# Kernel tuning notes

Measured on AMD Instinct MI355X. Metric: run time of the kernel, lower is better.

The kernel has to match this reference:

```python
import jax, jax.numpy as jnp
import numpy as np

N_NODES = 50000
N_EDGES = 800000
D_IN = 128
D_OUT = 128


def setup_inputs() -> dict:
    key = jax.random.key(0)
    k1, k2, k3, k4 = jax.random.split(key, 4)
    node_features = jax.random.normal(k1, (N_NODES, D_IN), dtype=jnp.float32)
    edge_index = jax.random.randint(k2, (2, N_EDGES), 0, N_NODES, dtype=jnp.int64)
    # nn.Linear params: weight [out, in], bias [out]
    W = jax.random.normal(k3, (D_OUT, D_IN), dtype=jnp.float32) / np.sqrt(D_IN)
    b = jax.random.normal(k4, (D_OUT,), dtype=jnp.float32) * 0.01
    return {"node_features": node_features, "edge_index": edge_index, "W": W, "b": b}


def reference(node_features, edge_index, W, b):
    source_nodes = edge_index[0]
    dest_nodes = edge_index[1]
    # gather neighbor features [E, D_in], scatter-add into [N, D_in]
    neighbor_features = node_features[source_nodes]
    aggregated = jax.ops.segment_sum(neighbor_features, dest_nodes,
                                     num_segments=node_features.shape[0])
    # nn.Linear: x @ W.T + b
    return aggregated @ W.T + b
```

## Files before the change

### kernel.cpp

```cpp
#include <hip/hip_runtime.h>


constexpr int NN = 50000;
constexpr int NE = 800000;
constexpr int D  = 128;

constexpr int BS  = 128;
constexpr int NB  = (NN + BS - 1) / BS;
constexpr int CAP = 4096;
constexpr int EPB = 4096;
constexpr int NBLK_B = (NE + EPB - 1) / EPB;

constexpr int AROWU = 136;

typedef __attribute__((ext_vector_type(8))) short bf16x8;
typedef __attribute__((ext_vector_type(4))) float f32x4;

__device__ inline unsigned short f2bf(float f) {
    unsigned u = __float_as_uint(f);
    return (unsigned short)((u + 0x7fffu + ((u >> 16) & 1u)) >> 16);
}
__device__ inline float bflo(unsigned v) { return __uint_as_float(v << 16); }
__device__ inline float bfhi(unsigned v) { return __uint_as_float(v & 0xffff0000u); }

constexpr int NF4 = NN * D / 4;
constexpr int W4  = D * D / 4;
constexpr int NBLK_P = (NF4 + W4 + 255) / 256;
constexpr int GRID_A = NBLK_B + NBLK_P;

__global__ __launch_bounds__(256) void k_prep_bucket(
    const float* __restrict__ nf, const float* __restrict__ W,
    const int* __restrict__ ei,
    ushort* __restrict__ nfh, ushort* __restrict__ Wh,
    int* __restrict__ cursor, unsigned* __restrict__ buf)
{
    __shared__ int h[NB];
    __shared__ int gbase[NB];
    __shared__ int lcur[NB];
    const int t = threadIdx.x;

    if (blockIdx.x < NBLK_B) {
        for (int i = t; i < NB; i += 256) { h[i] = 0; lcur[i] = 0; }
        __syncthreads();
        const int e0 = blockIdx.x * EPB;
        unsigned pk[16];
        #pragma unroll
        for (int j = 0; j < 16; ++j) {
            int e = e0 + j * 256 + t;
            if (e < NE) {
                unsigned s = (unsigned)ei[e];
                unsigned d = (unsigned)ei[NE + e];
                pk[j] = (d << 16) | s;
                atomicAdd(&h[pk[j] >> 23], 1);
            }
        }
        __syncthreads();
        for (int i = t; i < NB; i += 256)
            if (h[i] > 0) gbase[i] = i * CAP + atomicAdd(&cursor[i], h[i]);
        __syncthreads();
        #pragma unroll
        for (int j = 0; j < 16; ++j) {
            int e = e0 + j * 256 + t;
            if (e < NE) {
                unsigned b = pk[j] >> 23;
                int l = atomicAdd(&lcur[b], 1);
                buf[gbase[b] + l] = pk[j];
            }
        }
    } else {
        int i = (blockIdx.x - NBLK_B) * 256 + t;
        if (i < NF4) {
            float4 v = ((const float4*)nf)[i];
            ((ushort4*)nfh)[i] = make_ushort4(f2bf(v.x), f2bf(v.y), f2bf(v.z), f2bf(v.w));
        } else if (i < NF4 + W4) {
            int k = i - NF4;
            float4 v = ((const float4*)W)[k];
            ((ushort4*)Wh)[k] = make_ushort4(f2bf(v.x), f2bf(v.y), f2bf(v.z), f2bf(v.w));
        }
    }
}

__global__ __launch_bounds__(1024) void k_sort_agg(
    const unsigned* __restrict__ nfh, const unsigned* __restrict__ buf,
    const int* __restrict__ cursor, const ushort* __restrict__ Wh,
    const float* __restrict__ bias, float* __restrict__ out)
{
    __shared__ ushort srt[CAP];
    __shared__ int hist[BS], off[BS], cur[BS];
    __shared__ unsigned tile[BS * AROWU / 2];
    const int b = blockIdx.x, t = threadIdx.x;
    const int lane = t & 63, w = t >> 6;

    int cnt = cursor[b]; if (cnt > CAP) cnt = CAP;
    const unsigned* mybuf = buf + (size_t)b * CAP;

    if (t < BS) hist[t] = 0;
    __syncthreads();
    for (int e = t; e < cnt; e += 1024)
        atomicAdd(&hist[(mybuf[e] >> 16) & (BS - 1)], 1);
    __syncthreads();
    if (t < BS) off[t] = hist[t];
    __syncthreads();
    for (int o = 1; o < BS; o <<= 1) {
        int v = (t >= o && t < BS) ? off[t - o] : 0;
        __syncthreads();
        if (t < BS) off[t] += v;
        __syncthreads();
    }
    if (t < BS) { int ex = off[t] - hist[t]; off[t] = ex; cur[t] = ex; }
    __syncthreads();
    for (int e = t; e < cnt; e += 1024) {
        unsigned pk = mybuf[e];
        int n = (pk >> 16) & (BS - 1);
        int p = atomicAdd(&cur[n], 1);
        srt[p] = (ushort)(pk & 0xffffu);
    }
    __syncthreads();

    #pragma unroll
    for (int i = 0; i < 8; ++i) {
        const int n = w * 8 + i;
        const int beg = off[n], e = beg + hist[n];
        float ax=0.f, ay=0.f, bx=0.f, by=0.f, cx=0.f, cy=0.f, dx=0.f, dy=0.f;
        for (int p = beg; p < e; p += 8) {
            const int lim = e - 1;
            unsigned v[8];
            #pragma unroll
            for (int j = 0; j < 8; ++j) {
                int pos = p + j;
                bool ok = pos <= lim;
                if (!ok) pos = lim;
                unsigned s = srt[pos];
                unsigned val = nfh[(size_t)s * 64 + lane];
                v[j] = ok ? val : 0u;
            }
            ax += bflo(v[0]); ay += bfhi(v[0]);
            bx += bflo(v[1]); by += bfhi(v[1]);
            cx += bflo(v[2]); cy += bfhi(v[2]);
            dx += bflo(v[3]); dy += bfhi(v[3]);
            ax += bflo(v[4]); ay += bfhi(v[4]);
            bx += bflo(v[5]); by += bfhi(v[5]);
            cx += bflo(v[6]); cy += bfhi(v[6]);
            dx += bflo(v[7]); dy += bfhi(v[7]);
        }
        float rx = (ax + bx) + (cx + dx);
        float ry = (ay + by) + (cy + dy);
        tile[n * (AROWU / 2) + lane] =
            (unsigned)f2bf(rx) | ((unsigned)f2bf(ry) << 16);
    }
    __syncthreads();

    const int m = lane & 15, q = lane >> 4;
    const ushort* lds = (const ushort*)tile;
    #pragma unroll
    for (int i = 0; i < 4; ++i) {
        const int task = w + 16 * i;
        const int t16  = task >> 3;
        const int c0   = (task & 7) * 16;
        const int grow0 = b * BS + t16 * 16;
        if (grow0 < NN) {
            bf16x8 a[4];
            const ushort* arow = lds + (t16 * 16 + m) * AROWU + q * 8;
            #pragma unroll
            for (int kk = 0; kk < 4; ++kk)
                a[kk] = *(const bf16x8*)(arow + kk * 32);
            float bv = bias[c0 + m];
            f32x4 acc = { bv, bv, bv, bv };
            const ushort* wrow = Wh + (size_t)(c0 + m) * D + q * 8;
            #pragma unroll
            for (int kk = 0; kk < 4; ++kk) {
                bf16x8 bb = *(const bf16x8*)(wrow + kk * 32);
                acc = __builtin_amdgcn_mfma_f32_16x16x32_bf16(a[kk], bb, acc, 0, 0, 0);
            }
            float* op = out + (size_t)(grow0 + q * 4) * D + c0 + m;
            op[0]     = acc[0];
            op[D]     = acc[1];
            op[2 * D] = acc[2];
            op[3 * D] = acc[3];
        }
    }
}

extern "C" void kernel_launch(void* const* d_in, const int* in_sizes, int n_in,
                              void* d_out, int out_size, void* d_ws, size_t ws_size,
                              hipStream_t stream) {
    const float* nf = (const float*)d_in[0];
    const int*   ei = (const int*)d_in[1];
    const float* W  = (const float*)d_in[2];
    const float* b  = (const float*)d_in[3];
    float* out = (float*)d_out;

    ushort*   nfh    = (ushort*)d_ws;
    ushort*   Wh     = nfh + (size_t)NN * D;
    unsigned* buf    = (unsigned*)(Wh + D * D);
    int*      cursor = (int*)(buf + (size_t)NB * CAP);

    hipMemsetAsync(cursor, 0, NB * sizeof(int), stream);
    k_prep_bucket<<<GRID_A, 256, 0, stream>>>(nf, W, ei, nfh, Wh, cursor, buf);
    k_sort_agg   <<<NB, 1024, 0, stream>>>((const unsigned*)nfh, buf, cursor, Wh, b, out);
}
```

Baseline: 145.8 us.

## Replace global-cursor bucketing with fixed per-block sub-slots and consumer-side prefix scan

After: 140.7 us. -3.5%, faster.

```diff
diff --git a/kernel.cpp b/kernel.cpp
--- a/kernel.cpp
+++ b/kernel.cpp
@@ -5,11 +5,12 @@
 constexpr int NE = 800000;
 constexpr int D  = 128;
 
-constexpr int BS  = 128;
-constexpr int NB  = (NN + BS - 1) / BS;
-constexpr int CAP = 4096;
-constexpr int EPB = 4096;
-constexpr int NBLK_B = (NE + EPB - 1) / EPB;
+constexpr int BS   = 128;
+constexpr int NB   = (NN + BS - 1) / BS;
+constexpr int EPB  = 2048;
+constexpr int NSB  = (NE + EPB - 1) / EPB;
+constexpr int SUBCAP = 32;
+constexpr int CAP  = 4096;
 
 constexpr int AROWU = 136;
 
@@ -26,49 +27,40 @@
 constexpr int NF4 = NN * D / 4;
 constexpr int W4  = D * D / 4;
 constexpr int NBLK_P = (NF4 + W4 + 255) / 256;
-constexpr int GRID_A = NBLK_B + NBLK_P;
+constexpr int GRID_A = NSB + NBLK_P;
 
 __global__ __launch_bounds__(256) void k_prep_bucket(
     const float* __restrict__ nf, const float* __restrict__ W,
     const int* __restrict__ ei,
     ushort* __restrict__ nfh, ushort* __restrict__ Wh,
-    int* __restrict__ cursor, unsigned* __restrict__ buf)
+    ushort* __restrict__ cnt, unsigned* __restrict__ buf)
 {
-    __shared__ int h[NB];
-    __shared__ int gbase[NB];
     __shared__ int lcur[NB];
     const int t = threadIdx.x;
 
-    if (blockIdx.x < NBLK_B) {
-        for (int i = t; i < NB; i += 256) { h[i] = 0; lcur[i] = 0; }
-        __syncthreads();
-        const int e0 = blockIdx.x * EPB;
-        unsigned pk[16];
+    if (blockIdx.x < NSB) {
+        const int blk = blockIdx.x;
+        for (int i = t; i < NB; i += 256) lcur[i] = 0;
+        __syncthreads();
+        const int e0 = blk * EPB;
         #pragma unroll
-        for (int j = 0; j < 16; ++j) {
+        for (int j = 0; j < 8; ++j) {
             int e = e0 + j * 256 + t;
             if (e < NE) {
                 unsigned s = (unsigned)ei[e];
                 unsigned d = (unsigned)ei[NE + e];
-                pk[j] = (d << 16) | s;
-                atomicAdd(&h[pk[j] >> 23], 1);
+                unsigned pk = (d << 16) | s;
+                int bk = pk >> 23;
+                int l = atomicAdd(&lcur[bk], 1);
+                if (l < SUBCAP)
+                    buf[((size_t)bk * NSB + blk) * SUBCAP + l] = pk;
             }
         }
         __syncthreads();
         for (int i = t; i < NB; i += 256)
-            if (h[i] > 0) gbase[i] = i * CAP + atomicAdd(&cursor[i], h[i]);
-        __syncthreads();
-        #pragma unroll
-        for (int j = 0; j < 16; ++j) {
-            int e = e0 + j * 256 + t;
-            if (e < NE) {
-                unsigned b = pk[j] >> 23;
-                int l = atomicAdd(&lcur[b], 1);
-                buf[gbase[b] + l] = pk[j];
-            }
-        }
+            cnt[blk * NB + i] = (ushort)(lcur[i] < SUBCAP ? lcur[i] : SUBCAP);
     } else {
-        int i = (blockIdx.x - NBLK_B) * 256 + t;
+        int i = (blockIdx.x - NSB) * 256 + t;
         if (i < NF4) {
             float4 v = ((const float4*)nf)[i];
             ((ushort4*)nfh)[i] = make_ushort4(f2bf(v.x), f2bf(v.y), f2bf(v.z), f2bf(v.w));
@@ -82,23 +74,46 @@
 
 __global__ __launch_bounds__(1024) void k_sort_agg(
     const unsigned* __restrict__ nfh, const unsigned* __restrict__ buf,
-    const int* __restrict__ cursor, const ushort* __restrict__ Wh,
+    const ushort* __restrict__ cnt, const ushort* __restrict__ Wh,
     const float* __restrict__ bias, float* __restrict__ out)
 {
+    __shared__ unsigned pkbuf[CAP];
     __shared__ ushort srt[CAP];
+    __shared__ int scnt[512];
+    __shared__ int sbase[NSB];
     __shared__ int hist[BS], off[BS], cur[BS];
     __shared__ unsigned tile[BS * AROWU / 2];
     const int b = blockIdx.x, t = threadIdx.x;
     const int lane = t & 63, w = t >> 6;
 
-    int cnt = cursor[b]; if (cnt > CAP) cnt = CAP;
-    const unsigned* mybuf = buf + (size_t)b * CAP;
-
+    int my = 0;
+    if (t < NSB) my = (int)cnt[t * NB + b];
+    if (t < 512) scnt[t] = (t < NSB) ? my : 0;
+    __syncthreads();
+    for (int o = 1; o < 512; o <<= 1) {
+        int v = (t >= o && t < 512) ? scnt[t - o] : 0;
+        __syncthreads();
+        if (t < 512) scnt[t] += v;
+        __syncthreads();
+    }
+    if (t < NSB) sbase[t] = scnt[t] - my;
     if (t < BS) hist[t] = 0;
     __syncthreads();
-    for (int e = t; e < cnt; e += 1024)
-        atomicAdd(&hist[(mybuf[e] >> 16) & (BS - 1)], 1);
-    __syncthreads();
+    int total = scnt[NSB - 1];
+    if (total > CAP) total = CAP;
+
+    for (int p = t; p < total; p += 1024) {
+        int lo = 0, hi = NSB - 1;
+        while (lo < hi) {
+            int mid = (lo + hi) >> 1;
+            if (scnt[mid] > p) hi = mid; else lo = mid + 1;
+        }
+        unsigned pk = buf[((size_t)b * NSB + lo) * SUBCAP + (p - sbase[lo])];
+        pkbuf[p] = pk;
+        atomicAdd(&hist[(pk >> 16) & (BS - 1)], 1);
+    }
+    __syncthreads();
+
     if (t < BS) off[t] = hist[t];
     __syncthreads();
     for (int o = 1; o < BS; o <<= 1) {
@@ -109,8 +124,8 @@
     }
     if (t < BS) { int ex = off[t] - hist[t]; off[t] = ex; cur[t] = ex; }
     __syncthreads();
-    for (int e = t; e < cnt; e += 1024) {
-        unsigned pk = mybuf[e];
+    for (int e = t; e < total; e += 1024) {
+        unsigned pk = pkbuf[e];
         int n = (pk >> 16) & (BS - 1);
         int p = atomicAdd(&cur[n], 1);
         srt[p] = (ushort)(pk & 0xffffu);
@@ -190,12 +205,11 @@
     const float* b  = (const float*)d_in[3];
     float* out = (float*)d_out;
 
-    ushort*   nfh    = (ushort*)d_ws;
-    ushort*   Wh     = nfh + (size_t)NN * D;
-    unsigned* buf    = (unsigned*)(Wh + D * D);
-    int*      cursor = (int*)(buf + (size_t)NB * CAP);
-
-    hipMemsetAsync(cursor, 0, NB * sizeof(int), stream);
-    k_prep_bucket<<<GRID_A, 256, 0, stream>>>(nf, W, ei, nfh, Wh, cursor, buf);
-    k_sort_agg   <<<NB, 1024, 0, stream>>>((const unsigned*)nfh, buf, cursor, Wh, b, out);
-}
+    ushort*   nfh = (ushort*)d_ws;
+    ushort*   Wh  = nfh + (size_t)NN * D;
+    unsigned* buf = (unsigned*)(Wh + D * D);
+    ushort*   cnt = (ushort*)(buf + (size_t)NB * NSB * SUBCAP);
+
+    k_prep_bucket<<<GRID_A, 256, 0, stream>>>(nf, W, ei, nfh, Wh, cnt, buf);
+    k_sort_agg   <<<NB, 1024, 0, stream>>>((const unsigned*)nfh, buf, cnt, Wh, b, out);
+}
```
